# Kernel tuning notes

Measured on AMD Instinct MI355X. Metric: run time of the kernel, lower is better.

Reference implementation:

```python
import jax, jax.numpy as jnp
import numpy as np

TOP_K = 30
NUM_RBF = 16
EDGE_F = 128
NODE_F = 128
MAXREL = 32
EDGE_IN = NUM_RBF * 25  # 400


def _normalize(x, eps=1e-12):
    n = jnp.linalg.norm(x, axis=-1, keepdims=True)
    return x / jnp.maximum(n, eps)


def _rbf(D):
    # D: [..., ] distances -> [..., NUM_RBF]
    mu = jnp.linspace(2.0, 22.0, NUM_RBF)
    sigma = (22.0 - 2.0) / NUM_RBF
    return jnp.exp(-(((D[..., None] - mu) / sigma) ** 2))


def _layer_norm(x, g, b, eps=1e-5):
    m = x.mean(-1, keepdims=True)
    v = ((x - m) ** 2).mean(-1, keepdims=True)
    return (x - m) / jnp.sqrt(v + eps) * g + b


def setup_inputs() -> dict:
    key = jax.random.key(0)
    ks = jax.random.split(key, 8)
    B, L = 8, 1024
    X = jax.random.normal(ks[0], (B, L, 5, 3), jnp.float32) * 3.0  # backbone coords
    mask = jnp.ones((B, L), jnp.float32)
    Lvec = jnp.full((B,), L, dtype=jnp.int32)
    W_edge = jax.random.normal(ks[1], (EDGE_IN, EDGE_F), jnp.float32) * 0.05
    W_node = jax.random.normal(ks[2], (6, NODE_F), jnp.float32) * 0.05
    W_pos = jax.random.normal(ks[3], (2 * MAXREL + 1, EDGE_F), jnp.float32) * 0.05
    b_pos = jnp.zeros((EDGE_F,), jnp.float32)
    g_edge = jnp.ones((EDGE_F,), jnp.float32)
    b_edge = jnp.zeros((EDGE_F,), jnp.float32)
    g_node = jnp.ones((NODE_F,), jnp.float32)
    b_node = jnp.zeros((NODE_F,), jnp.float32)
    return {"X": X, "mask": mask, "Lvec": Lvec, "W_edge": W_edge, "W_node": W_node,
            "W_pos": W_pos, "b_pos": b_pos, "g_edge": g_edge, "b_edge": b_edge,
            "g_node": g_node, "b_node": b_node}


def reference(X, mask, Lvec, W_edge, W_node, W_pos, b_pos, g_edge, b_edge, g_node, b_node):
    B, L = X.shape[0], X.shape[1]
    N, Ca, C, CB, O = (X[:, :, i, :] for i in range(5))

    # backbone frames (4x4: rotation rows e1,e2,e3; translation Ca; bottom row zeros)
    v1 = C - Ca
    v2 = N - Ca
    e1 = _normalize(v1)
    u2 = v2 - e1 * jnp.sum(e1 * v2, axis=-1, keepdims=True)
    e2 = _normalize(u2)
    e3 = jnp.cross(e1, e2)
    R = jnp.stack([e1, e2, e3], axis=-2)  # [B,L,3,3]
    bb = jnp.zeros((B, L, 4, 4), X.dtype).at[..., :3, :3].set(R).at[..., :3, 3].set(Ca)

    # _dist: masked Ca-Ca pairwise distance + kNN
    mask2 = mask[:, None, :] * mask[:, :, None]  # [B,L,L]
    dX = Ca[:, :, None, :] - Ca[:, None, :, :]
    D = mask2 * jnp.sqrt(jnp.sum(dX ** 2, -1) + 1e-6)
    D_max = jnp.max(D, -1, keepdims=True)
    D_adjust = D + (1.0 - mask2) * D_max
    k = min(TOP_K, L)
    negD, E_idx = jax.lax.top_k(-D_adjust, k)  # smallest-k distances
    D_neighbors = -negD  # [B,L,K]

    # RBFs: compute distances only at selected neighbors (same math as full cdist+gather)
    bidx = jnp.arange(B)[:, None, None]

    def get_rbf(A, Bc):
        Bnb = Bc[bidx, E_idx]  # [B,L,K,3]
        d = jnp.sqrt(jnp.sum((A[:, :, None, :] - Bnb) ** 2, -1) + 1e-6)
        return _rbf(d)

    pairs = [(N, N), (C, C), (O, O), (CB, CB), (Ca, N), (Ca, C), (Ca, O), (Ca, CB),
             (N, C), (N, O), (N, CB), (CB, C), (CB, O), (O, C), (N, Ca), (C, Ca),
             (O, Ca), (CB, Ca), (C, N), (O, N), (CB, N), (C, CB), (O, CB), (C, O)]
    RBF_all = jnp.concatenate([_rbf(D_neighbors)] + [get_rbf(a, b) for a, b in pairs], axis=-1)  # [B,L,K,400]

    # positional encodings over sequence offsets of selected neighbors
    offset = jnp.arange(L)[None, :, None] - E_idx  # residue_idx[i] - residue_idx[j]
    d_clip = jnp.clip(offset + MAXREL, 0, 2 * MAXREL)
    E_pos = jax.nn.one_hot(d_clip, 2 * MAXREL + 1, dtype=X.dtype) @ W_pos + b_pos

    # dihedrals (phi, psi, omega) from N/CA/C chain
    X3 = X[:, :, :3, :].reshape(B, 3 * L, 3)
    dXc = X3[:, 1:, :] - X3[:, :-1, :]
    U = _normalize(dXc)
    u_2, u_1, u_0 = U[:, :-2, :], U[:, 1:-1, :], U[:, 2:, :]
    n_2 = _normalize(jnp.cross(u_2, u_1))
    n_1 = _normalize(jnp.cross(u_1, u_0))
    cosD = jnp.clip(jnp.sum(n_2 * n_1, -1), -1 + 1e-7, 1 - 1e-7)
    Dang = jnp.sign(jnp.sum(u_2 * n_1, -1)) * jnp.arccos(cosD)
    Dang = jnp.pad(Dang, ((0, 0), (1, 2))).reshape(B, L, 3)
    V = jnp.concatenate([jnp.cos(Dang), jnp.sin(Dang)], -1)  # [B,L,6]

    E = _layer_norm(RBF_all @ W_edge + E_pos, g_edge, b_edge)
    V = _layer_norm(V @ W_node, g_node, b_node)
    return (V, E, E_idx, bb)
```

## Files before the change

kernel.cpp:

```cpp
#include <hip/hip_runtime.h>
#include <hip/hip_bf16.h>
#include <math.h>

#define V_OFF    ((size_t)0)
#define E_OFF    ((size_t)1048576)
#define EIDX_OFF ((size_t)32505856)
#define BB_OFF   ((size_t)32751616)

#define K 30
#define NRBF 16
#define AH   232
#define SSTR 132

typedef __attribute__((ext_vector_type(8))) short bf16x8;
typedef __attribute__((ext_vector_type(4))) float f32x4;

__device__ __constant__ int c_pairA[24] = {0,2,4,3,1,1,1,1,0,0,0,3,3,4,0,2,4,3,2,4,3,2,4,2};
__device__ __constant__ int c_pairB[24] = {0,2,4,3,0,2,4,3,2,4,3,2,4,2,1,1,1,1,0,0,0,3,3,4};

__device__ __constant__ float c_muS[16] = {
    1.92179871f, 3.20299785f, 4.48419699f, 5.76539613f, 7.04659527f, 8.32779441f,
    9.60899355f, 10.89019269f, 12.17139183f, 13.45259097f, 14.73379011f, 16.01498925f,
    17.29618839f, 18.57738753f, 19.85858667f, 21.13978581f};

__device__ __forceinline__ unsigned short f2bu(float f) {
    unsigned x = __float_as_uint(f);
    return (unsigned short)((x + 0x7fffu + ((x >> 16) & 1u)) >> 16);
}

__device__ __forceinline__ unsigned wave_umin64(unsigned x) {
    unsigned t;
    t = __builtin_amdgcn_update_dpp(x, x, 0x111, 0xf, 0xf, false); x = min(x, t);
    t = __builtin_amdgcn_update_dpp(x, x, 0x112, 0xf, 0xf, false); x = min(x, t);
    t = __builtin_amdgcn_update_dpp(x, x, 0x114, 0xf, 0xf, false); x = min(x, t);
    t = __builtin_amdgcn_update_dpp(x, x, 0x118, 0xf, 0xf, false); x = min(x, t);
    t = __builtin_amdgcn_update_dpp(x, x, 0x142, 0xf, 0xf, false); x = min(x, t);
    t = __builtin_amdgcn_update_dpp(x, x, 0x143, 0xf, 0xf, false); x = min(x, t);
    return (unsigned)__builtin_amdgcn_readlane((int)x, 63);
}
__device__ __forceinline__ unsigned wave_umax64(unsigned x) {
    unsigned t;
    t = __builtin_amdgcn_update_dpp(x, x, 0x111, 0xf, 0xf, false); x = max(x, t);
    t = __builtin_amdgcn_update_dpp(x, x, 0x112, 0xf, 0xf, false); x = max(x, t);
    t = __builtin_amdgcn_update_dpp(x, x, 0x114, 0xf, 0xf, false); x = max(x, t);
    t = __builtin_amdgcn_update_dpp(x, x, 0x118, 0xf, 0xf, false); x = max(x, t);
    t = __builtin_amdgcn_update_dpp(x, x, 0x142, 0xf, 0xf, false); x = max(x, t);
    t = __builtin_amdgcn_update_dpp(x, x, 0x143, 0xf, 0xf, false); x = max(x, t);
    return (unsigned)__builtin_amdgcn_readlane((int)x, 63);
}
__device__ __forceinline__ float wave_fadd64(float x) {
    float t;
    t = __int_as_float(__builtin_amdgcn_update_dpp(0, __float_as_int(x), 0x111, 0xf, 0xf, true)); x += t;
    t = __int_as_float(__builtin_amdgcn_update_dpp(0, __float_as_int(x), 0x112, 0xf, 0xf, true)); x += t;
    t = __int_as_float(__builtin_amdgcn_update_dpp(0, __float_as_int(x), 0x114, 0xf, 0xf, true)); x += t;
    t = __int_as_float(__builtin_amdgcn_update_dpp(0, __float_as_int(x), 0x118, 0xf, 0xf, true)); x += t;
    t = __int_as_float(__builtin_amdgcn_update_dpp(0, __float_as_int(x), 0x142, 0xf, 0xf, true)); x += t;
    t = __int_as_float(__builtin_amdgcn_update_dpp(0, __float_as_int(x), 0x143, 0xf, 0xf, true)); x += t;
    return __int_as_float(__builtin_amdgcn_readlane(__float_as_int(x), 63));
}
__device__ __forceinline__ unsigned mbcnt64(unsigned long long m) {
    return __builtin_amdgcn_mbcnt_hi((unsigned)(m >> 32),
           __builtin_amdgcn_mbcnt_lo((unsigned)m, 0u));
}
__device__ __forceinline__ float group8_fadd(float x) {
    float t;
    t = __int_as_float(__builtin_amdgcn_update_dpp(__float_as_int(x), __float_as_int(x), 0x0B1, 0xf, 0xf, false)); x += t;
    t = __int_as_float(__builtin_amdgcn_update_dpp(__float_as_int(x), __float_as_int(x), 0x04E, 0xf, 0xf, false)); x += t;
    t = __int_as_float(__builtin_amdgcn_update_dpp(__float_as_int(x), __float_as_int(x), 0x141, 0xf, 0xf, false)); x += t;
    return x;
}

__device__ __forceinline__ void norm_to(const float v[3], float o[3]) {
    float n = sqrtf(v[0]*v[0] + v[1]*v[1] + v[2]*v[2]);
    n = fmaxf(n, 1e-12f);
    o[0] = v[0]/n; o[1] = v[1]/n; o[2] = v[2]/n;
}
__device__ __forceinline__ void unit_diff(const float a[3], const float b[3], float o[3]) {
    float v[3] = {a[0]-b[0], a[1]-b[1], a[2]-b[2]};
    norm_to(v, o);
}
__device__ __forceinline__ void cross_unit(const float a[3], const float b[3], float o[3]) {
    float c[3] = {a[1]*b[2]-a[2]*b[1], a[2]*b[0]-a[0]*b[2], a[0]*b[1]-a[1]*b[0]};
    norm_to(c, o);
}

__global__ __launch_bounds__(256) void prep_kernel(
    const float* __restrict__ We, unsigned short* __restrict__ Wb,
    unsigned* __restrict__ rtab, const float* __restrict__ X,
    float4* __restrict__ ca4)
{
    const int bid = blockIdx.x, tid = threadIdx.x;
    if (bid < 13) {
        if (tid < 128) {
            const int s = bid, j = tid;
            unsigned* dst = (unsigned*)(Wb + ((size_t)(s*128 + j) << 5));
            #pragma unroll
            for (int m = 0; m < 16; ++m) {
                const int k0 = s*32 + 2*m;
                const unsigned lo = (k0   < 400) ? f2bu(We[(size_t)k0*128 + j])     : 0u;
                const unsigned hi = (k0+1 < 400) ? f2bu(We[(size_t)(k0+1)*128 + j]) : 0u;
                dst[m] = (hi << 16) | lo;
            }
        }
    } else if (bid < 29) {
        const int idx = (bid - 13)*256 + tid;
        const float t1 = (idx * 0.02f) * 0.96089935f;
        unsigned* dst = rtab + ((size_t)idx << 3);
        #pragma unroll
        for (int m = 0; m < 8; ++m) {
            const float z0 = t1 - c_muS[2*m];
            const float z1 = t1 - c_muS[2*m+1];
            const float v0 = exp2f(-z0*z0);
            const float v1 = exp2f(-z1*z1);
            unsigned pk;
            asm("v_cvt_pk_bf16_f32 %0, %1, %2" : "=v"(pk) : "v"(v0), "v"(v1));
            dst[m] = pk;
        }
    } else {
        const int idx = (bid - 29)*256 + tid;
        const float* p = X + (size_t)idx*15;
        ca4[idx] = make_float4(p[3], p[4], p[5], 0.f);
    }
}

__global__ __launch_bounds__(256, 8) void topk_edge_kernel(
    const float* __restrict__ X, const float* __restrict__ mask,
    const unsigned short* __restrict__ Wb, const float* __restrict__ Wp,
    const float* __restrict__ bp, const float* __restrict__ ge,
    const float* __restrict__ be, const float4* __restrict__ ca4,
    const unsigned* __restrict__ rtab,
    const float* __restrict__ Wn, const float* __restrict__ gn,
    const float* __restrict__ bn, float* __restrict__ out)
{
    const int blk = blockIdx.x;
    const int b = blk >> 10, i = blk & 1023;
    const int tid = threadIdx.x;
    const int w = tid >> 6, lane = tid & 63;

    __shared__ __align__(16) unsigned char uni_raw[K * SSTR * 4];
    __shared__ float redf4[4];
    __shared__ unsigned redT[4];
    __shared__ int   scount;
    __shared__ float nbA[K][15];
    __shared__ int   nj[K];
    __shared__ float dnbv[K];
    __shared__ float angf[3];
    unsigned short* A_lds = (unsigned short*)uni_raw;
    float* S = (float*)uni_raw;
    unsigned long long* surv = (unsigned long long*)uni_raw;

    if (tid == 0) scount = 0;

    const float4 me = ca4[(b << 10) + i];
    const float mi  = mask[(b << 10) + i];

    float dv_r[4], m2_r[4];
    float lmax = -1.f;
    #pragma unroll
    for (int m = 0; m < 4; ++m) {
        const int j = tid + (m << 8);
        const float4 cj = ca4[(b << 10) + j];
        const float dx = __fsub_rn(me.x, cj.x);
        const float dy = __fsub_rn(me.y, cj.y);
        const float dz = __fsub_rn(me.z, cj.z);
        const float ss = __fadd_rn(__fadd_rn(__fmul_rn(dx,dx), __fmul_rn(dy,dy)), __fmul_rn(dz,dz));
        const float dist = __fsqrt_rn(__fadd_rn(ss, 1e-6f));
        const float m2 = __fmul_rn(mi, mask[(b << 10) + j]);
        const float Dv = __fmul_rn(m2, dist);
        dv_r[m] = Dv; m2_r[m] = m2;
        lmax = fmaxf(lmax, Dv);
    }
    const float wmax = __uint_as_float(wave_umax64(__float_as_uint(lmax)));
    if (lane == 0) redf4[w] = wmax;
    __syncthreads();
    const float Dmax = fmaxf(fmaxf(redf4[0], redf4[1]), fmaxf(redf4[2], redf4[3]));

    unsigned va[4];
    #pragma unroll
    for (int m = 0; m < 4; ++m)
        va[m] = __float_as_uint(__fadd_rn(dv_r[m], __fmul_rn(__fsub_rn(1.f, m2_r[m]), Dmax)));

    {
        unsigned a0 = va[0], a1 = va[1];
        unsigned b0 = va[2], b1 = va[3];
        unsigned vA = 0, vB = 0;
        #pragma unroll
        for (int k = 0; k < 4; ++k) {
            const unsigned hA = min(a0, a1);
            const unsigned hB = min(b0, b1);
            vA = wave_umin64(hA);
            vB = wave_umin64(hB);
            a0 = (a0 == vA) ? 0xffffffffu : a0;
            a1 = (a1 == vA) ? 0xffffffffu : a1;
            b0 = (b0 == vB) ? 0xffffffffu : b0;
            b1 = (b1 == vB) ? 0xffffffffu : b1;
        }
        if (lane == 0) redT[w] = max(vA, vB);
    }
    __syncthreads();
    const unsigned T = max(max(redT[0], redT[1]), max(redT[2], redT[3]));

    {
        unsigned long long mm0 = __ballot(va[0] <= T);
        unsigned long long mm1 = __ballot(va[1] <= T);
        unsigned long long mm2 = __ballot(va[2] <= T);
        unsigned long long mm3 = __ballot(va[3] <= T);
        const unsigned c0 = __popcll(mm0), c1 = __popcll(mm1);
        const unsigned c2 = __popcll(mm2), c3 = __popcll(mm3);
        int old = 0;
        if (lane == 0) old = atomicAdd(&scount, (int)(c0 + c1 + c2 + c3));
        unsigned base = (unsigned)__builtin_amdgcn_readfirstlane(old);
        if (va[0] <= T) surv[base + mbcnt64(mm0)] = ((unsigned long long)va[0] << 32) | (unsigned)tid;
        base += c0;
        if (va[1] <= T) surv[base + mbcnt64(mm1)] = ((unsigned long long)va[1] << 32) | (unsigned)(tid + 256);
        base += c1;
        if (va[2] <= T) surv[base + mbcnt64(mm2)] = ((unsigned long long)va[2] << 32) | (unsigned)(tid + 512);
        base += c2;
        if (va[3] <= T) surv[base + mbcnt64(mm3)] = ((unsigned long long)va[3] << 32) | (unsigned)(tid + 768);
    }
    __syncthreads();
    const int N = scount;

    for (int base = 0; base < N; base += 256) {
        const int t = base + tid;
        if (t < N) {
            const unsigned long long mykey = surv[t];
            int rank = 0;
            #pragma unroll 4
            for (int u = 0; u < N; ++u) rank += (surv[u] < mykey) ? 1 : 0;
            if (rank < K) {
                const int j = (int)(mykey & 0xffffffffu);
                nj[rank] = j;
                dnbv[rank] = __uint_as_float((unsigned)(mykey >> 32));
                out[EIDX_OFF + (size_t)blk * K + rank] = (float)j;
            }
        }
    }
    __syncthreads();

    for (int t = tid; t < K*15; t += 256) {
        const int e = t / 15, r = t - e*15;
        nbA[e][r] = X[((size_t)(b << 10) + nj[e])*15 + r];
    }
    __syncthreads();

    const float* sa = X + (size_t)blk * 15;
    f32x4 acc00 = {0,0,0,0}, acc01 = {0,0,0,0}, acc10 = {0,0,0,0}, acc11 = {0,0,0,0};
    const int ar = lane & 15;
    const int kg = (lane >> 4) * 8;
    const unsigned short* a_base = A_lds + ar*AH + kg;
    const unsigned short* a_base1 = a_base + 16*AH;
    const unsigned short* b_base = Wb + ((size_t)(w*32 + ar) << 5) + kg;

    for (int t = tid; t < K*12; t += 256) {
        const int e = t / 12, g = t - e*12;
        float d;
        if (g == 0) d = dnbv[e];
        else {
            const int p = g - 1;
            const int aA = c_pairA[p], aB = c_pairB[p];
            const float dx = sa[aA*3+0] - nbA[e][aB*3+0];
            const float dy = sa[aA*3+1] - nbA[e][aB*3+1];
            const float dz = sa[aA*3+2] - nbA[e][aB*3+2];
            d = sqrtf(dx*dx + dy*dy + dz*dz + 1e-6f);
        }
        int idx = (int)__fmaf_rn(d, 50.f, 0.5f);
        idx = min(idx, 4095);
        const uint4* src = (const uint4*)(rtab + ((size_t)idx << 3));
        uint4* dst = (uint4*)(A_lds + e*AH + g*NRBF);
        dst[0] = src[0]; dst[1] = src[1];
    }
    __syncthreads();
    #pragma unroll
    for (int s = 0; s < 6; ++s) {
        const bf16x8 a0 = *reinterpret_cast<const bf16x8*>(a_base + s*32);
        const bf16x8 a1 = *reinterpret_cast<const bf16x8*>(a_base1 + s*32);
        const bf16x8 b0 = *reinterpret_cast<const bf16x8*>(b_base + (size_t)s*4096);
        const bf16x8 b1 = *reinterpret_cast<const bf16x8*>(b_base + (size_t)s*4096 + 512);
        acc00 = __builtin_amdgcn_mfma_f32_16x16x32_bf16(a0, b0, acc00, 0, 0, 0);
        acc01 = __builtin_amdgcn_mfma_f32_16x16x32_bf16(a0, b1, acc01, 0, 0, 0);
        acc10 = __builtin_amdgcn_mfma_f32_16x16x32_bf16(a1, b0, acc10, 0, 0, 0);
        acc11 = __builtin_amdgcn_mfma_f32_16x16x32_bf16(a1, b1, acc11, 0, 0, 0);
    }
    __syncthreads();

    for (int t = tid; t < K*13; t += 256) {
        const int e = t / 13, gg = t - e*13;
        const int p = 11 + gg;
        const int aA = c_pairA[p], aB = c_pairB[p];
        const float dx = sa[aA*3+0] - nbA[e][aB*3+0];
        const float dy = sa[aA*3+1] - nbA[e][aB*3+1];
        const float dz = sa[aA*3+2] - nbA[e][aB*3+2];
        const float d = sqrtf(dx*dx + dy*dy + dz*dz + 1e-6f);
        int idx = (int)__fmaf_rn(d, 50.f, 0.5f);
        idx = min(idx, 4095);
        const uint4* src = (const uint4*)(rtab + ((size_t)idx << 3));
        uint4* dst = (uint4*)(A_lds + e*AH + gg*NRBF);
        dst[0] = src[0]; dst[1] = src[1];
    }
    for (int t = tid; t < K*8; t += 256) {
        const int e = t >> 3, c = t & 7;
        ((unsigned*)(A_lds + e*AH + 208))[c] = 0u;
    }
    __syncthreads();
    #pragma unroll
    for (int s = 0; s < 7; ++s) {
        const bf16x8 a0 = *reinterpret_cast<const bf16x8*>(a_base + s*32);
        const bf16x8 a1 = *reinterpret_cast<const bf16x8*>(a_base1 + s*32);
        const bf16x8 b0 = *reinterpret_cast<const bf16x8*>(b_base + (size_t)(6+s)*4096);
        const bf16x8 b1 = *reinterpret_cast<const bf16x8*>(b_base + (size_t)(6+s)*4096 + 512);
        acc00 = __builtin_amdgcn_mfma_f32_16x16x32_bf16(a0, b0, acc00, 0, 0, 0);
        acc01 = __builtin_amdgcn_mfma_f32_16x16x32_bf16(a0, b1, acc01, 0, 0, 0);
        acc10 = __builtin_amdgcn_mfma_f32_16x16x32_bf16(a1, b0, acc10, 0, 0, 0);
        acc11 = __builtin_amdgcn_mfma_f32_16x16x32_bf16(a1, b1, acc11, 0, 0, 0);
    }
    __syncthreads();

    {
        const int crow = (lane >> 4) * 4;
        const int ccol = w*32 + (lane & 15);
        const float bp0 = bp[ccol], bp1 = bp[ccol + 16];
        #pragma unroll
        for (int r = 0; r < 4; ++r) {
            const int r0 = crow + r;
            if (r0 < K) {
                int off = i - nj[r0] + 32;
                off = off < 0 ? 0 : (off > 64 ? 64 : off);
                const float* wr = Wp + (size_t)off*128;
                S[r0*SSTR + ccol]      = acc00[r] + (wr[ccol]      + bp0);
                S[r0*SSTR + ccol + 16] = acc01[r] + (wr[ccol + 16] + bp1);
            }
            const int r1 = 16 + crow + r;
            if (r1 < K) {
                int off = i - nj[r1] + 32;
                off = off < 0 ? 0 : (off > 64 ? 64 : off);
                const float* wr = Wp + (size_t)off*128;
                S[r1*SSTR + ccol]      = acc10[r] + (wr[ccol]      + bp0);
                S[r1*SSTR + ccol + 16] = acc11[r] + (wr[ccol + 16] + bp1);
            }
        }
    }
    __syncthreads();

    {
        const int e = tid >> 3, s8 = tid & 7;
        if (e < K) {
            const float* row = S + e*SSTR + s8*16;
            float xv[16];
            float sum = 0.f;
            #pragma unroll
            for (int c = 0; c < 4; ++c) {
                const float4 q = ((const float4*)row)[c];
                xv[4*c+0] = q.x; xv[4*c+1] = q.y; xv[4*c+2] = q.z; xv[4*c+3] = q.w;
                sum += q.x + q.y + q.z + q.w;
            }
            const float mean = group8_fadd(sum) * (1.f/128.f);
            float vs = 0.f;
            #pragma unroll
            for (int c = 0; c < 16; ++c) { const float d = xv[c] - mean; xv[c] = d; vs = __fmaf_rn(d, d, vs); }
            const float inv = 1.f / __fsqrt_rn(group8_fadd(vs) * (1.f/128.f) + 1e-5f);
            const int j0 = s8*16;
            float* op = out + E_OFF + ((size_t)blk * K + e) * 128 + j0;
            #pragma unroll
            for (int c = 0; c < 4; ++c) {
                const float4 g4 = ((const float4*)(ge + j0))[c];
                const float4 b4 = ((const float4*)(be + j0))[c];
                float4 o;
                o.x = xv[4*c+0] * inv * g4.x + b4.x;
                o.y = xv[4*c+1] * inv * g4.y + b4.y;
                o.z = xv[4*c+2] * inv * g4.z + b4.z;
                o.w = xv[4*c+3] * inv * g4.w + b4.w;
                ((float4*)op)[c] = o;
            }
        }
    }

    if (tid < 3) {
        const int m = 3*i + tid;
        float dang = 0.f;
        if (m >= 1 && m <= 3*1024 - 3) {
            const int t = m - 1;
            float P[4][3];
            #pragma unroll
            for (int q = 0; q < 4; ++q) {
                const int s = t + q;
                const int ri = s / 3, ai = s - 3*ri;
                const float* p = X + (((size_t)b * 1024 + ri) * 5 + ai) * 3;
                P[q][0] = p[0]; P[q][1] = p[1]; P[q][2] = p[2];
            }
            float u2v[3], u1v[3], u0v[3];
            unit_diff(P[1], P[0], u2v);
            unit_diff(P[2], P[1], u1v);
            unit_diff(P[3], P[2], u0v);
            float n2v[3], n1v[3];
            cross_unit(u2v, u1v, n2v);
            cross_unit(u1v, u0v, n1v);
            float cosD = n2v[0]*n1v[0] + n2v[1]*n1v[1] + n2v[2]*n1v[2];
            cosD = fminf(fmaxf(cosD, -1.f + 1e-7f), 1.f - 1e-7f);
            float sg = u2v[0]*n1v[0] + u2v[1]*n1v[1] + u2v[2]*n1v[2];
            float s = (sg > 0.f) ? 1.f : ((sg < 0.f) ? -1.f : 0.f);
            dang = s * acosf(cosD);
        }
        angf[tid] = dang;
    }
    if (tid == 3) {
        float Nx=sa[0],  Ny=sa[1],  Nz=sa[2];
        float Cax=sa[3], Cay=sa[4], Caz=sa[5];
        float Cx=sa[6],  Cy=sa[7],  Cz=sa[8];
        float v1[3] = {Cx-Cax, Cy-Cay, Cz-Caz};
        float v2[3] = {Nx-Cax, Ny-Cay, Nz-Caz};
        float e1[3]; norm_to(v1, e1);
        float dd = e1[0]*v2[0] + e1[1]*v2[1] + e1[2]*v2[2];
        float u2[3] = {v2[0]-e1[0]*dd, v2[1]-e1[1]*dd, v2[2]-e1[2]*dd};
        float e2[3]; norm_to(u2, e2);
        float e3[3] = {e1[1]*e2[2]-e1[2]*e2[1], e1[2]*e2[0]-e1[0]*e2[2], e1[0]*e2[1]-e1[1]*e2[0]};
        float* bb = out + BB_OFF + (size_t)blk * 16;
        bb[0]=e1[0]; bb[1]=e1[1]; bb[2]=e1[2];  bb[3]=Cax;
        bb[4]=e2[0]; bb[5]=e2[1]; bb[6]=e2[2];  bb[7]=Cay;
        bb[8]=e3[0]; bb[9]=e3[1]; bb[10]=e3[2]; bb[11]=Caz;
        bb[12]=0.f; bb[13]=0.f; bb[14]=0.f; bb[15]=0.f;
    }
    __syncthreads();
    float xV = 0.f;
    if (tid < 128) {
        const float a0 = angf[0], a1 = angf[1], a2 = angf[2];
        const float feat[6] = {cosf(a0), cosf(a1), cosf(a2), sinf(a0), sinf(a1), sinf(a2)};
        #pragma unroll
        for (int f = 0; f < 6; ++f) xV += feat[f] * Wn[f*128 + tid];
        const float s = wave_fadd64(xV);
        if (lane == 0) redf4[w] = s;
    }
    __syncthreads();
    float xm = 0.f;
    if (tid < 128) {
        const float mean = (redf4[0] + redf4[1]) * (1.f/128.f);
        xm = xV - mean;
        const float vsum = wave_fadd64(xm*xm);
        if (lane == 0) redT[w] = __float_as_uint(vsum);
    }
    __syncthreads();
    if (tid < 128) {
        const float var = (__uint_as_float(redT[0]) + __uint_as_float(redT[1])) * (1.f/128.f);
        out[V_OFF + (size_t)blk * 128 + tid] = xm / __fsqrt_rn(var + 1e-5f) * gn[tid] + bn[tid];
    }
}

extern "C" void kernel_launch(void* const* d_in, const int* in_sizes, int n_in,
                              void* d_out, int out_size, void* d_ws, size_t ws_size,
                              hipStream_t stream) {
    const float* X    = (const float*)d_in[0];
    const float* mask = (const float*)d_in[1];
    const float* We   = (const float*)d_in[3];
    const float* Wn   = (const float*)d_in[4];
    const float* Wp   = (const float*)d_in[5];
    const float* bp   = (const float*)d_in[6];
    const float* gE   = (const float*)d_in[7];
    const float* bE   = (const float*)d_in[8];
    const float* gN   = (const float*)d_in[9];
    const float* bN   = (const float*)d_in[10];
    float* out = (float*)d_out;
    unsigned short* Wb = (unsigned short*)d_ws;
    float4* ca4 = (float4*)((char*)d_ws + 106496);
    unsigned* rtab = (unsigned*)((char*)d_ws + 106496 + 131072);

    hipLaunchKernelGGL(prep_kernel,      dim3(61),   dim3(256), 0, stream, We, Wb, rtab, X, ca4);
    hipLaunchKernelGGL(topk_edge_kernel, dim3(8192), dim3(256), 0, stream,
                       X, mask, Wb, Wp, bp, gE, bE, ca4, rtab, Wn, gN, bN, out);
}
```

Measured before the change: 131.3 us.

## Use 512-thread blocks, splitting per-row work across eight waves

```diff
diff --git a/kernel.cpp b/kernel.cpp
--- a/kernel.cpp
+++ b/kernel.cpp
@@ -62,11 +62,12 @@
     return __builtin_amdgcn_mbcnt_hi((unsigned)(m >> 32),
            __builtin_amdgcn_mbcnt_lo((unsigned)m, 0u));
 }
-__device__ __forceinline__ float group8_fadd(float x) {
+__device__ __forceinline__ float group16_fadd(float x) {
     float t;
     t = __int_as_float(__builtin_amdgcn_update_dpp(__float_as_int(x), __float_as_int(x), 0x0B1, 0xf, 0xf, false)); x += t;
     t = __int_as_float(__builtin_amdgcn_update_dpp(__float_as_int(x), __float_as_int(x), 0x04E, 0xf, 0xf, false)); x += t;
     t = __int_as_float(__builtin_amdgcn_update_dpp(__float_as_int(x), __float_as_int(x), 0x141, 0xf, 0xf, false)); x += t;
+    t = __int_as_float(__builtin_amdgcn_update_dpp(__float_as_int(x), __float_as_int(x), 0x140, 0xf, 0xf, false)); x += t;
     return x;
 }
 
@@ -123,7 +124,7 @@
     }
 }
 
-__global__ __launch_bounds__(256, 8) void topk_edge_kernel(
+__global__ __launch_bounds__(512, 8) void topk_edge_kernel(
     const float* __restrict__ X, const float* __restrict__ mask,
     const unsigned short* __restrict__ Wb, const float* __restrict__ Wp,
     const float* __restrict__ bp, const float* __restrict__ ge,
@@ -138,8 +139,8 @@
     const int w = tid >> 6, lane = tid & 63;
 
     __shared__ __align__(16) unsigned char uni_raw[K * SSTR * 4];
-    __shared__ float redf4[4];
-    __shared__ unsigned redT[4];
+    __shared__ float redf8[8];
+    __shared__ unsigned redT8[8];
     __shared__ int   scount;
     __shared__ float nbA[K][15];
     __shared__ int   nj[K];
@@ -154,11 +155,11 @@
     const float4 me = ca4[(b << 10) + i];
     const float mi  = mask[(b << 10) + i];
 
-    float dv_r[4], m2_r[4];
+    float dv_r[2], m2_r[2];
     float lmax = -1.f;
     #pragma unroll
-    for (int m = 0; m < 4; ++m) {
-        const int j = tid + (m << 8);
+    for (int m = 0; m < 2; ++m) {
+        const int j = tid + (m << 9);
         const float4 cj = ca4[(b << 10) + j];
         const float dx = __fsub_rn(me.x, cj.x);
         const float dy = __fsub_rn(me.y, cj.y);
@@ -171,57 +172,47 @@
         lmax = fmaxf(lmax, Dv);
     }
     const float wmax = __uint_as_float(wave_umax64(__float_as_uint(lmax)));
-    if (lane == 0) redf4[w] = wmax;
-    __syncthreads();
-    const float Dmax = fmaxf(fmaxf(redf4[0], redf4[1]), fmaxf(redf4[2], redf4[3]));
-
-    unsigned va[4];
-    #pragma unroll
-    for (int m = 0; m < 4; ++m)
+    if (lane == 0) redf8[w] = wmax;
+    __syncthreads();
+    float Dmax = redf8[0];
+    #pragma unroll
+    for (int q = 1; q < 8; ++q) Dmax = fmaxf(Dmax, redf8[q]);
+
+    unsigned va[2];
+    #pragma unroll
+    for (int m = 0; m < 2; ++m)
         va[m] = __float_as_uint(__fadd_rn(dv_r[m], __fmul_rn(__fsub_rn(1.f, m2_r[m]), Dmax)));
 
     {
-        unsigned a0 = va[0], a1 = va[1];
-        unsigned b0 = va[2], b1 = va[3];
-        unsigned vA = 0, vB = 0;
-        #pragma unroll
-        for (int k = 0; k < 4; ++k) {
-            const unsigned hA = min(a0, a1);
-            const unsigned hB = min(b0, b1);
-            vA = wave_umin64(hA);
-            vB = wave_umin64(hB);
-            a0 = (a0 == vA) ? 0xffffffffu : a0;
-            a1 = (a1 == vA) ? 0xffffffffu : a1;
-            b0 = (b0 == vB) ? 0xffffffffu : b0;
-            b1 = (b1 == vB) ? 0xffffffffu : b1;
-        }
-        if (lane == 0) redT[w] = max(vA, vB);
-    }
-    __syncthreads();
-    const unsigned T = max(max(redT[0], redT[1]), max(redT[2], redT[3]));
+        unsigned a0 = va[0], b0 = va[1];
+        const unsigned vA1 = wave_umin64(a0);
+        const unsigned vB1 = wave_umin64(b0);
+        a0 = (a0 == vA1) ? 0xffffffffu : a0;
+        b0 = (b0 == vB1) ? 0xffffffffu : b0;
+        const unsigned vA2 = wave_umin64(a0);
+        const unsigned vB2 = wave_umin64(b0);
+        if (lane == 0) redT8[w] = max(vA2, vB2);
+    }
+    __syncthreads();
+    unsigned T = redT8[0];
+    #pragma unroll
+    for (int q = 1; q < 8; ++q) T = max(T, redT8[q]);
 
     {
         unsigned long long mm0 = __ballot(va[0] <= T);
         unsigned long long mm1 = __ballot(va[1] <= T);
-        unsigned long long mm2 = __ballot(va[2] <= T);
-        unsigned long long mm3 = __ballot(va[3] <= T);
         const unsigned c0 = __popcll(mm0), c1 = __popcll(mm1);
-        const unsigned c2 = __popcll(mm2), c3 = __popcll(mm3);
         int old = 0;
-        if (lane == 0) old = atomicAdd(&scount, (int)(c0 + c1 + c2 + c3));
+        if (lane == 0) old = atomicAdd(&scount, (int)(c0 + c1));
         unsigned base = (unsigned)__builtin_amdgcn_readfirstlane(old);
         if (va[0] <= T) surv[base + mbcnt64(mm0)] = ((unsigned long long)va[0] << 32) | (unsigned)tid;
         base += c0;
-        if (va[1] <= T) surv[base + mbcnt64(mm1)] = ((unsigned long long)va[1] << 32) | (unsigned)(tid + 256);
-        base += c1;
-        if (va[2] <= T) surv[base + mbcnt64(mm2)] = ((unsigned long long)va[2] << 32) | (unsigned)(tid + 512);
-        base += c2;
-        if (va[3] <= T) surv[base + mbcnt64(mm3)] = ((unsigned long long)va[3] << 32) | (unsigned)(tid + 768);
+        if (va[1] <= T) surv[base + mbcnt64(mm1)] = ((unsigned long long)va[1] << 32) | (unsigned)(tid + 512);
     }
     __syncthreads();
     const int N = scount;
 
-    for (int base = 0; base < N; base += 256) {
+    for (int base = 0; base < N; base += 512) {
         const int t = base + tid;
         if (t < N) {
             const unsigned long long mykey = surv[t];
@@ -238,22 +229,22 @@
     }
     __syncthreads();
 
-    for (int t = tid; t < K*15; t += 256) {
-        const int e = t / 15, r = t - e*15;
+    if (tid < K*15) {
+        const int e = tid / 15, r = tid - e*15;
         nbA[e][r] = X[((size_t)(b << 10) + nj[e])*15 + r];
     }
     __syncthreads();
 
     const float* sa = X + (size_t)blk * 15;
-    f32x4 acc00 = {0,0,0,0}, acc01 = {0,0,0,0}, acc10 = {0,0,0,0}, acc11 = {0,0,0,0};
+    f32x4 acc0 = {0,0,0,0}, acc1 = {0,0,0,0};
     const int ar = lane & 15;
     const int kg = (lane >> 4) * 8;
     const unsigned short* a_base = A_lds + ar*AH + kg;
     const unsigned short* a_base1 = a_base + 16*AH;
-    const unsigned short* b_base = Wb + ((size_t)(w*32 + ar) << 5) + kg;
-
-    for (int t = tid; t < K*12; t += 256) {
-        const int e = t / 12, g = t - e*12;
+    const unsigned short* b_base = Wb + ((size_t)(w*16 + ar) << 5) + kg;
+
+    if (tid < K*12) {
+        const int e = tid / 12, g = tid - e*12;
         float d;
         if (g == 0) d = dnbv[e];
         else {
@@ -273,19 +264,16 @@
     __syncthreads();
     #pragma unroll
     for (int s = 0; s < 6; ++s) {
-        const bf16x8 a0 = *reinterpret_cast<const bf16x8*>(a_base + s*32);
-        const bf16x8 a1 = *reinterpret_cast<const bf16x8*>(a_base1 + s*32);
-        const bf16x8 b0 = *reinterpret_cast<const bf16x8*>(b_base + (size_t)s*4096);
-        const bf16x8 b1 = *reinterpret_cast<const bf16x8*>(b_base + (size_t)s*4096 + 512);
-        acc00 = __builtin_amdgcn_mfma_f32_16x16x32_bf16(a0, b0, acc00, 0, 0, 0);
-        acc01 = __builtin_amdgcn_mfma_f32_16x16x32_bf16(a0, b1, acc01, 0, 0, 0);
-        acc10 = __builtin_amdgcn_mfma_f32_16x16x32_bf16(a1, b0, acc10, 0, 0, 0);
-        acc11 = __builtin_amdgcn_mfma_f32_16x16x32_bf16(a1, b1, acc11, 0, 0, 0);
-    }
-    __syncthreads();
-
-    for (int t = tid; t < K*13; t += 256) {
-        const int e = t / 13, gg = t - e*13;
+        const bf16x8 a0v = *reinterpret_cast<const bf16x8*>(a_base + s*32);
+        const bf16x8 a1v = *reinterpret_cast<const bf16x8*>(a_base1 + s*32);
+        const bf16x8 b0v = *reinterpret_cast<const bf16x8*>(b_base + (size_t)s*4096);
+        acc0 = __builtin_amdgcn_mfma_f32_16x16x32_bf16(a0v, b0v, acc0, 0, 0, 0);
+        acc1 = __builtin_amdgcn_mfma_f32_16x16x32_bf16(a1v, b0v, acc1, 0, 0, 0);
+    }
+    __syncthreads();
+
+    if (tid < K*13) {
+        const int e = tid / 13, gg = tid - e*13;
         const int p = 11 + gg;
         const int aA = c_pairA[p], aB = c_pairB[p];
         const float dx = sa[aA*3+0] - nbA[e][aB*3+0];
@@ -298,71 +286,64 @@
         uint4* dst = (uint4*)(A_lds + e*AH + gg*NRBF);
         dst[0] = src[0]; dst[1] = src[1];
     }
-    for (int t = tid; t < K*8; t += 256) {
-        const int e = t >> 3, c = t & 7;
+    if (tid < K*8) {
+        const int e = tid >> 3, c = tid & 7;
         ((unsigned*)(A_lds + e*AH + 208))[c] = 0u;
     }
     __syncthreads();
     #pragma unroll
     for (int s = 0; s < 7; ++s) {
-        const bf16x8 a0 = *reinterpret_cast<const bf16x8*>(a_base + s*32);
-        const bf16x8 a1 = *reinterpret_cast<const bf16x8*>(a_base1 + s*32);
-        const bf16x8 b0 = *reinterpret_cast<const bf16x8*>(b_base + (size_t)(6+s)*4096);
-        const bf16x8 b1 = *reinterpret_cast<const bf16x8*>(b_base + (size_t)(6+s)*4096 + 512);
-        acc00 = __builtin_amdgcn_mfma_f32_16x16x32_bf16(a0, b0, acc00, 0, 0, 0);
-        acc01 = __builtin_amdgcn_mfma_f32_16x16x32_bf16(a0, b1, acc01, 0, 0, 0);
-        acc10 = __builtin_amdgcn_mfma_f32_16x16x32_bf16(a1, b0, acc10, 0, 0, 0);
-        acc11 = __builtin_amdgcn_mfma_f32_16x16x32_bf16(a1, b1, acc11, 0, 0, 0);
+        const bf16x8 a0v = *reinterpret_cast<const bf16x8*>(a_base + s*32);
+        const bf16x8 a1v = *reinterpret_cast<const bf16x8*>(a_base1 + s*32);
+        const bf16x8 b0v = *reinterpret_cast<const bf16x8*>(b_base + (size_t)(6+s)*4096);
+        acc0 = __builtin_amdgcn_mfma_f32_16x16x32_bf16(a0v, b0v, acc0, 0, 0, 0);
+        acc1 = __builtin_amdgcn_mfma_f32_16x16x32_bf16(a1v, b0v, acc1, 0, 0, 0);
     }
     __syncthreads();
 
     {
         const int crow = (lane >> 4) * 4;
-        const int ccol = w*32 + (lane & 15);
-        const float bp0 = bp[ccol], bp1 = bp[ccol + 16];
+        const int ccol = w*16 + ar;
+        const float bp0 = bp[ccol];
         #pragma unroll
         for (int r = 0; r < 4; ++r) {
             const int r0 = crow + r;
             if (r0 < K) {
                 int off = i - nj[r0] + 32;
                 off = off < 0 ? 0 : (off > 64 ? 64 : off);
-                const float* wr = Wp + (size_t)off*128;
-                S[r0*SSTR + ccol]      = acc00[r] + (wr[ccol]      + bp0);
-                S[r0*SSTR + ccol + 16] = acc01[r] + (wr[ccol + 16] + bp1);
+                S[r0*SSTR + ccol] = acc0[r] + (Wp[(size_t)off*128 + ccol] + bp0);
             }
             const int r1 = 16 + crow + r;
             if (r1 < K) {
                 int off = i - nj[r1] + 32;
                 off = off < 0 ? 0 : (off > 64 ? 64 : off);
-                const float* wr = Wp + (size_t)off*128;
-                S[r1*SSTR + ccol]      = acc10[r] + (wr[ccol]      + bp0);
-                S[r1*SSTR + ccol + 16] = acc11[r] + (wr[ccol + 16] + bp1);
+                S[r1*SSTR + ccol] = acc1[r] + (Wp[(size_t)off*128 + ccol] + bp0);
             }
         }
     }
     __syncthreads();
 
     {
-        const int e = tid >> 3, s8 = tid & 7;
+        const int e = tid >> 4, sub = tid & 15;
         if (e < K) {
-            const float* row = S + e*SSTR + s8*16;
-            float xv[16];
+            const int j0 = sub*8;
+            const float* row = S + e*SSTR + j0;
+            float xv[8];
             float sum = 0.f;
             #pragma unroll
-            for (int c = 0; c < 4; ++c) {
+            for (int c = 0; c < 2; ++c) {
                 const float4 q = ((const float4*)row)[c];
                 xv[4*c+0] = q.x; xv[4*c+1] = q.y; xv[4*c+2] = q.z; xv[4*c+3] = q.w;
                 sum += q.x + q.y + q.z + q.w;
             }
-            const float mean = group8_fadd(sum) * (1.f/128.f);
+            const float mean = group16_fadd(sum) * (1.f/128.f);
             float vs = 0.f;
             #pragma unroll
-            for (int c = 0; c < 16; ++c) { const float d = xv[c] - mean; xv[c] = d; vs = __fmaf_rn(d, d, vs); }
-            const float inv = 1.f / __fsqrt_rn(group8_fadd(vs) * (1.f/128.f) + 1e-5f);
-            const int j0 = s8*16;
+            for (int c = 0; c < 8; ++c) { const float d = xv[c] - mean; xv[c] = d; vs = __fmaf_rn(d, d, vs); }
+            const float inv = 1.f / __fsqrt_rn(group16_fadd(vs) * (1.f/128.f) + 1e-5f);
             float* op = out + E_OFF + ((size_t)blk * K + e) * 128 + j0;
             #pragma unroll
-            for (int c = 0; c < 4; ++c) {
+            for (int c = 0; c < 2; ++c) {
                 const float4 g4 = ((const float4*)(ge + j0))[c];
                 const float4 b4 = ((const float4*)(be + j0))[c];
                 float4 o;
@@ -428,19 +409,19 @@
         #pragma unroll
         for (int f = 0; f < 6; ++f) xV += feat[f] * Wn[f*128 + tid];
         const float s = wave_fadd64(xV);
-        if (lane == 0) redf4[w] = s;
+        if (lane == 0) redf8[w] = s;
     }
     __syncthreads();
     float xm = 0.f;
     if (tid < 128) {
-        const float mean = (redf4[0] + redf4[1]) * (1.f/128.f);
+        const float mean = (redf8[0] + redf8[1]) * (1.f/128.f);
         xm = xV - mean;
         const float vsum = wave_fadd64(xm*xm);
-        if (lane == 0) redT[w] = __float_as_uint(vsum);
+        if (lane == 0) redT8[w] = __float_as_uint(vsum);
     }
     __syncthreads();
     if (tid < 128) {
-        const float var = (__uint_as_float(redT[0]) + __uint_as_float(redT[1])) * (1.f/128.f);
+        const float var = (__uint_as_float(redT8[0]) + __uint_as_float(redT8[1])) * (1.f/128.f);
         out[V_OFF + (size_t)blk * 128 + tid] = xm / __fsqrt_rn(var + 1e-5f) * gn[tid] + bn[tid];
     }
 }
@@ -464,6 +445,6 @@
     unsigned* rtab = (unsigned*)((char*)d_ws + 106496 + 131072);
 
     hipLaunchKernelGGL(prep_kernel,      dim3(61),   dim3(256), 0, stream, We, Wb, rtab, X, ca4);
-    hipLaunchKernelGGL(topk_edge_kernel, dim3(8192), dim3(256), 0, stream,
+    hipLaunchKernelGGL(topk_edge_kernel, dim3(8192), dim3(512), 0, stream,
                        X, mask, Wb, Wp, bp, gE, bE, ca4, rtab, Wn, gN, bN, out);
 }
```

Measured after the change: 154.5 us. 1.18x slower.
